# Kernel tuning notes

Measured on AMD Instinct MI355X. Metric: run time of the kernel, lower is better.

The kernel has to match this reference:

```python
import jax, jax.numpy as jnp
import numpy as np

B, C1, C2, K, H, W = 2, 256, 256, 3, 64, 64
PAD = 1
EPS = 1e-5
K2 = K * K
OUT_OFF = 3 * K2  # deform_groups=1: 2*k2 offset channels + k2 mask channels


def setup_inputs() -> dict:
    key = jax.random.key(0)
    ks = jax.random.split(key, 8)
    x = jax.random.normal(ks[0], (B, C1, H, W), jnp.float32)
    # small scale so predicted offsets stay within a few pixels (realistic trained regime)
    w_off = jax.random.normal(ks[1], (OUT_OFF, C1, 3, 3), jnp.float32) * 0.01
    b_off = jax.random.normal(ks[2], (OUT_OFF,), jnp.float32) * 0.01
    w_dcn = jax.random.normal(ks[3], (C2, C1, K, K), jnp.float32) / np.sqrt(C1 * K2).astype(np.float32)
    gamma = 1.0 + 0.1 * jax.random.normal(ks[4], (C2,), jnp.float32)
    beta = 0.1 * jax.random.normal(ks[5], (C2,), jnp.float32)
    run_mean = 0.1 * jax.random.normal(ks[6], (C2,), jnp.float32)
    run_var = jax.random.uniform(ks[7], (C2,), jnp.float32, minval=0.5, maxval=1.5)
    return {"x": x, "w_off": w_off, "b_off": b_off, "w_dcn": w_dcn,
            "gamma": gamma, "beta": beta, "run_mean": run_mean, "run_var": run_var}


def _dcnv2_bn_silu(x, w_off, b_off, w_dcn, gamma, beta, run_mean, run_var):
    # offset/mask predictor: plain 3x3 conv, stride 1, pad 1
    om = jax.lax.conv_general_dilated(x, w_off, (1, 1), [(PAD, PAD), (PAD, PAD)])
    om = om + b_off[None, :, None, None]  # [B, 27, H, W]
    # mmcv channel layout: (dy, dx) interleaved per kernel tap, then mask
    offset = om[:, :2 * K2].reshape(B, K2, 2, H, W)
    mask = jax.nn.sigmoid(om[:, 2 * K2:3 * K2])  # [B, K2, H, W]
    dy, dx = offset[:, :, 0], offset[:, :, 1]     # [B, K2, H, W]

    ki = jnp.arange(K)
    tap_y = jnp.repeat(ki, K)  # [K2]
    tap_x = jnp.tile(ki, K)    # [K2]
    base_y = jnp.arange(H)[None, None, :, None] - PAD + tap_y[None, :, None, None]
    base_x = jnp.arange(W)[None, None, None, :] - PAD + tap_x[None, :, None, None]
    py = base_y.astype(x.dtype) + dy  # [B, K2, H, W] sampling rows
    px = base_x.astype(x.dtype) + dx  # [B, K2, H, W] sampling cols

    y0f = jnp.floor(py)
    x0f = jnp.floor(px)
    ly = (py - y0f)[:, None]  # [B, 1, K2, H, W]
    lx = (px - x0f)[:, None]
    y0 = y0f.astype(jnp.int32)
    x0 = x0f.astype(jnp.int32)

    x_flat = x.reshape(B, C1, H * W)

    def gather(yi, xi):
        valid = ((yi >= 0) & (yi < H) & (xi >= 0) & (xi < W)).astype(x.dtype)
        idx = jnp.clip(yi, 0, H - 1) * W + jnp.clip(xi, 0, W - 1)  # [B, K2, H, W]
        v = jnp.take_along_axis(x_flat, idx.reshape(B, 1, -1), axis=2)
        return v.reshape(B, C1, K2, H, W) * valid[:, None]

    v00 = gather(y0, x0)
    v01 = gather(y0, x0 + 1)
    v10 = gather(y0 + 1, x0)
    v11 = gather(y0 + 1, x0 + 1)
    vals = (v00 * (1 - ly) * (1 - lx) + v01 * (1 - ly) * lx
            + v10 * ly * (1 - lx) + v11 * ly * lx)
    vals = vals * mask[:, None]  # modulated

    out = jnp.einsum('bckhw,ock->bohw', vals, w_dcn.reshape(C2, C1, K2))

    # BatchNorm (inference, running stats) + SiLU
    inv = gamma / jnp.sqrt(run_var + EPS)
    y = out * inv[None, :, None, None] + (beta - run_mean * inv)[None, :, None, None]
    return y * jax.nn.sigmoid(y)


def reference(x, w_off, b_off, w_dcn, gamma, beta, run_mean, run_var):
    return _dcnv2_bn_silu(x, w_off, b_off, w_dcn, gamma, beta, run_mean, run_var)
```

## Files before the change

kernel.cpp:

```cpp
#include <hip/hip_runtime.h>
#include <hip/hip_bf16.h>
#include <math.h>

typedef __bf16 bf16x8 __attribute__((ext_vector_type(8)));
typedef float  f32x4  __attribute__((ext_vector_type(4)));

#define BB 2
#define C1 256
#define C2 256
#define HH 64
#define WW 64
#define HW 4096
#define OCH 27
#define EPSV 1e-5f

#define WBF_OFF  0u
#define WOFF_OFF 1179648u
#define XT_OFF   1327104u

__global__ __launch_bounds__(256) void prep_kernel(
    const float* __restrict__ x, const float* __restrict__ w_dcn,
    const float* __restrict__ w_off, __bf16* __restrict__ xT,
    __bf16* __restrict__ wbfS, __bf16* __restrict__ woffS)
{
    __shared__ __bf16 tile[64][72];
    __shared__ __bf16 lw[16][584];
    const int bi = blockIdx.x, tid = threadIdx.x;

    if (bi < 512) {
        const int b = bi >> 8;
        const int ht = (bi & 255) >> 2;
        const int ct = bi & 3;
        const int hw_l = tid & 63, cg = tid >> 6;
        const float* src = x + ((size_t)(b * 256 + ct * 64 + cg * 16) << 12)
                             + ht * 64 + hw_l;
        #pragma unroll
        for (int i = 0; i < 16; i++)
            tile[hw_l][cg * 16 + i] = (__bf16)src[(size_t)i << 12];
        __syncthreads();
        const int hw_o = tid >> 2, cq = tid & 3;
        __bf16* dst = xT + ((size_t)(b * HW + ht * 64 + hw_o) << 8)
                         + ct * 64 + cq * 16;
        *(bf16x8*)dst       = *(const bf16x8*)&tile[hw_o][cq * 16];
        *(bf16x8*)(dst + 8) = *(const bf16x8*)&tile[hw_o][cq * 16 + 8];
    } else if (bi < 576) {
        const int b2 = bi - 512;
        const int nb = b2 >> 2, qtr = b2 & 3;
        #pragma unroll
        for (int ii = 0; ii < 9; ii++) {
            int m = tid + 256 * ii;
            int base = m * 4;
            int o_l = base / 576;
            int f = base - o_l * 576;
            float4 v = *(const float4*)(w_dcn
                + (size_t)(nb * 16 + o_l) * 2304 + qtr * 576 + f);
            lw[o_l][f]     = (__bf16)v.x;
            lw[o_l][f + 1] = (__bf16)v.y;
            lw[o_l][f + 2] = (__bf16)v.z;
            lw[o_l][f + 3] = (__bf16)v.w;
        }
        __syncthreads();
        for (int p = tid; p < 1152; p += 256) {
            int lane = p & 63, seg = p >> 6;
            int tap = seg >> 1, ks = seg & 1;
            int kb = tap * 4 + qtr;
            int o_l = lane & 15, kq = (lane >> 4) & 3;
            bf16x8 v;
            #pragma unroll
            for (int j = 0; j < 8; j++)
                v[j] = lw[o_l][(ks * 32 + kq * 8 + j) * 9 + tap];
            *(bf16x8*)(wbfS
                + ((size_t)(((kb * 2 + ks) * 16 + nb) * 64 + lane)) * 8) = v;
        }
    } else {
        int t = (bi - 576) * 256 + tid;
        int l = t & 63;
        int nf = (t >> 6) & 1;
        int ks = (t >> 7) & 1;
        int kb = t >> 8;
        int o = nf * 16 + (l & 15);
        int kq = (l >> 4) & 3;
        bf16x8 v;
        #pragma unroll
        for (int j = 0; j < 8; j++) {
            int K = kb * 64 + ks * 32 + kq * 8 + j;
            v[j] = (o < OCH) ? (__bf16)w_off[o * 2304 + (K & 255) * 9 + (K >> 8)]
                             : (__bf16)0.f;
        }
        *(bf16x8*)(woffS + (size_t)t * 8) = v;
    }
}

union SU {
    float sD[8][2][16][33];
    float sC[4][32][133];
};

__global__ __launch_bounds__(512, 2) void fused_kernel(
    const __bf16* __restrict__ xT, const __bf16* __restrict__ wbfS,
    const __bf16* __restrict__ woffS, const float* __restrict__ b_off,
    const float* __restrict__ gamma, const float* __restrict__ beta,
    const float* __restrict__ rmean, const float* __restrict__ rvar,
    float* __restrict__ out)
{
    __shared__ SU u;
    __shared__ float  sOm[32][33];
    __shared__ int4   sO[9][32];
    __shared__ float4 sW[9][32];

    const int tid = threadIdx.x, wv = tid >> 6, lane = tid & 63;
    const int g = (blockIdx.x & 7) * 32 + (blockIdx.x >> 3);
    const int pixBase = g * 32;
    const int b = pixBase >> 12;
    const int hwBase = pixBase & 4095;
    const int h = hwBase >> 6, w0 = hwBase & 63;
    const int n15 = lane & 15, q4 = lane >> 4;

    const int cc  = wv >> 1;
    const int ksw = wv & 1;
    const char* xb = (const char*)xT + ((size_t)b << 12) * 512;
    const int chOffB = (cc * 64 + ksw * 32 + q4 * 8) * 2;

    {
        f32x4 acc2[2][2];
        #pragma unroll
        for (int nf = 0; nf < 2; nf++)
            #pragma unroll
            for (int t = 0; t < 2; t++)
                acc2[nf][t] = (f32x4){0.f, 0.f, 0.f, 0.f};

        #pragma unroll
        for (int k = 0; k < 9; k++) {
            const int kb = k * 4 + cc;
            const int kh = k / 3, kw = k % 3;
            const int hh = h + kh - 1;
            const int hc = min(max(hh, 0), HH - 1);
            const bool vy = (hh >= 0) && (hh < HH);
            bf16x8 af[2];
            #pragma unroll
            for (int t = 0; t < 2; t++) {
                const int ww = w0 + t * 16 + n15 + kw - 1;
                const bool valid = vy && (ww >= 0) && (ww < WW);
                const int wc = min(max(ww, 0), WW - 1);
                af[t] = *(const bf16x8*)(xb + (size_t)(hc * WW + wc) * 512
                                            + chOffB);
                if (!valid) {
                    #pragma unroll
                    for (int j = 0; j < 8; j++) af[t][j] = (__bf16)0.f;
                }
            }
            #pragma unroll
            for (int nf = 0; nf < 2; nf++) {
                bf16x8 bfr = *(const bf16x8*)(woffS
                    + ((size_t)(((kb * 2 + ksw) * 2 + nf) * 64 + lane)) * 8);
                #pragma unroll
                for (int t = 0; t < 2; t++)
                    acc2[nf][t] = __builtin_amdgcn_mfma_f32_16x16x32_bf16(
                        af[t], bfr, acc2[nf][t], 0, 0, 0);
            }
        }
        #pragma unroll
        for (int nf = 0; nf < 2; nf++)
            #pragma unroll
            for (int t = 0; t < 2; t++)
                #pragma unroll
                for (int r = 0; r < 4; r++)
                    u.sD[wv][t][q4 * 4 + r][nf * 16 + n15] = acc2[nf][t][r];
    }
    __syncthreads();
    for (int t2 = tid; t2 < OCH * 32; t2 += 512) {
        int oc = t2 >> 5, p = t2 & 31;
        float s = b_off[oc];
        #pragma unroll
        for (int w = 0; w < 8; w++) s += u.sD[w][p >> 4][p & 15][oc];
        sOm[oc][p] = s;
    }
    __syncthreads();

    if (tid < 288) {
        int k = tid >> 5, p = tid & 31;
        float dy = sOm[2 * k][p];
        float dx = sOm[2 * k + 1][p];
        float mm = sOm[18 + k][p];
        mm = 1.f / (1.f + __expf(-mm));
        float py = (float)(h - 1 + k / 3) + dy;
        float px = (float)(w0 + p - 1 + k % 3) + dx;
        float y0f = floorf(py), x0f = floorf(px);
        float ly = py - y0f, lx = px - x0f;
        int y0 = (int)y0f, x0 = (int)x0f;
        int yc0 = min(max(y0, 0), HH - 1),     yc1 = min(max(y0 + 1, 0), HH - 1);
        int xc0 = min(max(x0, 0), WW - 1),     xc1 = min(max(x0 + 1, 0), WW - 1);
        float vy0 = (y0 >= 0 && y0 < HH) ? 1.f : 0.f;
        float vy1 = (y0 + 1 >= 0 && y0 + 1 < HH) ? 1.f : 0.f;
        float vx0 = (x0 >= 0 && x0 < WW) ? 1.f : 0.f;
        float vx1 = (x0 + 1 >= 0 && x0 + 1 < WW) ? 1.f : 0.f;
        sO[k][p] = (int4){(yc0 * WW + xc0) * 512, (yc0 * WW + xc1) * 512,
                          (yc1 * WW + xc0) * 512, (yc1 * WW + xc1) * 512};
        sW[k][p] = (float4){(1.f - ly) * (1.f - lx) * vy0 * vx0 * mm,
                            (1.f - ly) * lx         * vy0 * vx1 * mm,
                            ly         * (1.f - lx) * vy1 * vx0 * mm,
                            ly         * lx         * vy1 * vx1 * mm};
    }
    __syncthreads();

    f32x4 acc[2][16];
    #pragma unroll
    for (int t = 0; t < 2; t++)
        #pragma unroll
        for (int j = 0; j < 16; j++) acc[t][j] = (f32x4){0.f, 0.f, 0.f, 0.f};

    const char* base = xb + chOffB;
    for (int k = 0; k < 9; k++) {
        const int kb = k * 4 + cc;
        const int4   O0 = sO[k][n15],      O1 = sO[k][16 + n15];
        const float4 W0 = sW[k][n15],      W1 = sW[k][16 + n15];

        bf16x8 a00 = *(const bf16x8*)(base + O0.x);
        bf16x8 a01 = *(const bf16x8*)(base + O0.y);
        bf16x8 a10 = *(const bf16x8*)(base + O0.z);
        bf16x8 a11 = *(const bf16x8*)(base + O0.w);
        bf16x8 b00 = *(const bf16x8*)(base + O1.x);
        bf16x8 b01 = *(const bf16x8*)(base + O1.y);
        bf16x8 b10 = *(const bf16x8*)(base + O1.z);
        bf16x8 b11 = *(const bf16x8*)(base + O1.w);

        bf16x8 af0, af1;
        #pragma unroll
        for (int j = 0; j < 8; j++) {
            float v0 = W0.x * (float)a00[j] + W0.y * (float)a01[j]
                     + W0.z * (float)a10[j] + W0.w * (float)a11[j];
            float v1 = W1.x * (float)b00[j] + W1.y * (float)b01[j]
                     + W1.z * (float)b10[j] + W1.w * (float)b11[j];
            af0[j] = (__bf16)v0;
            af1[j] = (__bf16)v1;
        }

        #pragma unroll
        for (int hf = 0; hf < 2; hf++) {
            bf16x8 bfr[8];
            #pragma unroll
            for (int nb = 0; nb < 8; nb++)
                bfr[nb] = *(const bf16x8*)(wbfS
                    + ((size_t)(((kb * 2 + ksw) * 16 + hf * 8 + nb) * 64 + lane)) * 8);
            #pragma unroll
            for (int nb = 0; nb < 8; nb++) {
                acc[0][hf * 8 + nb] = __builtin_amdgcn_mfma_f32_16x16x32_bf16(
                    af0, bfr[nb], acc[0][hf * 8 + nb], 0, 0, 0);
                acc[1][hf * 8 + nb] = __builtin_amdgcn_mfma_f32_16x16x32_bf16(
                    af1, bfr[nb], acc[1][hf * 8 + nb], 0, 0, 0);
            }
        }
    }

    #pragma unroll
    for (int pass = 0; pass < 2; pass++) {
        if (wv < 4) {
            #pragma unroll
            for (int t = 0; t < 2; t++)
                #pragma unroll
                for (int nb = 0; nb < 8; nb++)
                    #pragma unroll
                    for (int r = 0; r < 4; r++)
                        u.sC[wv][t * 16 + q4 * 4 + r][nb * 16 + n15]
                            = acc[t][pass * 8 + nb][r];
        }
        __syncthreads();
        if (wv >= 4) {
            #pragma unroll
            for (int t = 0; t < 2; t++)
                #pragma unroll
                for (int nb = 0; nb < 8; nb++)
                    #pragma unroll
                    for (int r = 0; r < 4; r++)
                        u.sC[wv - 4][t * 16 + q4 * 4 + r][nb * 16 + n15]
                            += acc[t][pass * 8 + nb][r];
        }
        __syncthreads();

        const int px = tid & 31, og = tid >> 5;
        #pragma unroll
        for (int ii = 0; ii < 8; ii++) {
            int col = og * 8 + ii;
            int o = pass * 128 + col;
            float s = u.sC[0][px][col] + u.sC[1][px][col]
                    + u.sC[2][px][col] + u.sC[3][px][col];
            float inv = gamma[o] * rsqrtf(rvar[o] + EPSV);
            float sh = beta[o] - rmean[o] * inv;
            float y = s * inv + sh;
            out[(size_t)((b * C2 + o) << 12) + hwBase + px]
                = y * (1.f / (1.f + __expf(-y)));
        }
        __syncthreads();
    }
}

extern "C" void kernel_launch(void* const* d_in, const int* in_sizes, int n_in,
                              void* d_out, int out_size, void* d_ws, size_t ws_size,
                              hipStream_t stream) {
    const float* x      = (const float*)d_in[0];
    const float* w_off  = (const float*)d_in[1];
    const float* b_off  = (const float*)d_in[2];
    const float* w_dcn  = (const float*)d_in[3];
    const float* gamma  = (const float*)d_in[4];
    const float* beta   = (const float*)d_in[5];
    const float* rmean  = (const float*)d_in[6];
    const float* rvar   = (const float*)d_in[7];
    float* out = (float*)d_out;

    char* ws = (char*)d_ws;
    __bf16* wbfS  = (__bf16*)(ws + WBF_OFF);
    __bf16* woffS = (__bf16*)(ws + WOFF_OFF);
    __bf16* xT    = (__bf16*)(ws + XT_OFF);

    prep_kernel<<<612, 256, 0, stream>>>(x, w_dcn, w_off, xT, wbfS, woffS);
    fused_kernel<<<256, 512, 0, stream>>>(xT, wbfS, woffS, b_off,
                                          gamma, beta, rmean, rvar, out);
}
```

Measured before the change: 121.1 us.

## Merge prep and fused kernels into one cooperative kernel with grid sync

Combines the layout/precision prep kernel and the main deformable-conv kernel into a single cooperative launch. Each of the 256 blocks first transposes its share of x to bf16, and some blocks also repack the weights. A grid-wide barrier follows, then the original fused compute runs. This removes one kernel launch and the gap between the two kernels. In exchange it adds a grid sync, and it requires all 256 blocks of 512 threads to be co-resident, which the cooperative launch enforces.

```diff
diff --git a/kernel.cpp b/kernel.cpp
--- a/kernel.cpp
+++ b/kernel.cpp
@@ -1,6 +1,9 @@
 #include <hip/hip_runtime.h>
 #include <hip/hip_bf16.h>
+#include <hip/hip_cooperative_groups.h>
 #include <math.h>
+
+namespace cg = cooperative_groups;
 
 typedef __bf16 bf16x8 __attribute__((ext_vector_type(8)));
 typedef float  f32x4  __attribute__((ext_vector_type(4)));
@@ -18,62 +21,83 @@
 #define WOFF_OFF 1179648u
 #define XT_OFF   1327104u
 
-__global__ __launch_bounds__(256) void prep_kernel(
-    const float* __restrict__ x, const float* __restrict__ w_dcn,
-    const float* __restrict__ w_off, __bf16* __restrict__ xT,
+union SU {
+    float  sD[8][2][16][33];
+    float  sC[4][32][133];
+    __bf16 tile[2][64][72];
+    __bf16 lw[16][584];
+};
+
+__global__ __launch_bounds__(512, 2) void mega_kernel(
+    const float* __restrict__ x, const float* __restrict__ w_off,
+    const float* __restrict__ w_dcn, const float* __restrict__ b_off,
+    const float* __restrict__ gamma, const float* __restrict__ beta,
+    const float* __restrict__ rmean, const float* __restrict__ rvar,
+    float* __restrict__ out, __bf16* __restrict__ xT,
     __bf16* __restrict__ wbfS, __bf16* __restrict__ woffS)
 {
-    __shared__ __bf16 tile[64][72];
-    __shared__ __bf16 lw[16][584];
-    const int bi = blockIdx.x, tid = threadIdx.x;
-
-    if (bi < 512) {
-        const int b = bi >> 8;
-        const int ht = (bi & 255) >> 2;
-        const int ct = bi & 3;
-        const int hw_l = tid & 63, cg = tid >> 6;
+    __shared__ SU u;
+    __shared__ float  sOm[32][33];
+    __shared__ int4   sO[9][32];
+    __shared__ float4 sW[9][32];
+
+    const int tid = threadIdx.x, bid = blockIdx.x;
+
+    {
+        const int sub = tid >> 8, t8 = tid & 255;
+        const int u2 = bid * 2 + sub;
+        const int b = u2 >> 8;
+        const int ht = (u2 & 255) >> 2;
+        const int ct = u2 & 3;
+        const int hw_l = t8 & 63, cg = t8 >> 6;
         const float* src = x + ((size_t)(b * 256 + ct * 64 + cg * 16) << 12)
                              + ht * 64 + hw_l;
         #pragma unroll
         for (int i = 0; i < 16; i++)
-            tile[hw_l][cg * 16 + i] = (__bf16)src[(size_t)i << 12];
-        __syncthreads();
-        const int hw_o = tid >> 2, cq = tid & 3;
+            u.tile[sub][hw_l][cg * 16 + i] = (__bf16)src[(size_t)i << 12];
+        __syncthreads();
+        const int hw_o = t8 >> 2, cq = t8 & 3;
         __bf16* dst = xT + ((size_t)(b * HW + ht * 64 + hw_o) << 8)
                          + ct * 64 + cq * 16;
-        *(bf16x8*)dst       = *(const bf16x8*)&tile[hw_o][cq * 16];
-        *(bf16x8*)(dst + 8) = *(const bf16x8*)&tile[hw_o][cq * 16 + 8];
-    } else if (bi < 576) {
-        const int b2 = bi - 512;
-        const int nb = b2 >> 2, qtr = b2 & 3;
-        #pragma unroll
-        for (int ii = 0; ii < 9; ii++) {
-            int m = tid + 256 * ii;
-            int base = m * 4;
-            int o_l = base / 576;
-            int f = base - o_l * 576;
-            float4 v = *(const float4*)(w_dcn
-                + (size_t)(nb * 16 + o_l) * 2304 + qtr * 576 + f);
-            lw[o_l][f]     = (__bf16)v.x;
-            lw[o_l][f + 1] = (__bf16)v.y;
-            lw[o_l][f + 2] = (__bf16)v.z;
-            lw[o_l][f + 3] = (__bf16)v.w;
-        }
-        __syncthreads();
-        for (int p = tid; p < 1152; p += 256) {
-            int lane = p & 63, seg = p >> 6;
-            int tap = seg >> 1, ks = seg & 1;
-            int kb = tap * 4 + qtr;
-            int o_l = lane & 15, kq = (lane >> 4) & 3;
-            bf16x8 v;
-            #pragma unroll
-            for (int j = 0; j < 8; j++)
-                v[j] = lw[o_l][(ks * 32 + kq * 8 + j) * 9 + tap];
-            *(bf16x8*)(wbfS
-                + ((size_t)(((kb * 2 + ks) * 16 + nb) * 64 + lane)) * 8) = v;
-        }
-    } else {
-        int t = (bi - 576) * 256 + tid;
+        *(bf16x8*)dst       = *(const bf16x8*)&u.tile[sub][hw_o][cq * 16];
+        *(bf16x8*)(dst + 8) = *(const bf16x8*)&u.tile[sub][hw_o][cq * 16 + 8];
+    }
+    __syncthreads();
+
+    if (bid < 64) {
+        const int nb = bid >> 2, qtr = bid & 3;
+        if (tid < 256) {
+            #pragma unroll
+            for (int ii = 0; ii < 9; ii++) {
+                int m = tid + 256 * ii;
+                int base = m * 4;
+                int o_l = base / 576;
+                int f = base - o_l * 576;
+                float4 v = *(const float4*)(w_dcn
+                    + (size_t)(nb * 16 + o_l) * 2304 + qtr * 576 + f);
+                u.lw[o_l][f]     = (__bf16)v.x;
+                u.lw[o_l][f + 1] = (__bf16)v.y;
+                u.lw[o_l][f + 2] = (__bf16)v.z;
+                u.lw[o_l][f + 3] = (__bf16)v.w;
+            }
+        }
+        __syncthreads();
+        if (tid < 256) {
+            for (int p = tid; p < 1152; p += 256) {
+                int lane = p & 63, seg = p >> 6;
+                int tap = seg >> 1, ks = seg & 1;
+                int kb = tap * 4 + qtr;
+                int o_l = lane & 15, kq = (lane >> 4) & 3;
+                bf16x8 v;
+                #pragma unroll
+                for (int j = 0; j < 8; j++)
+                    v[j] = u.lw[o_l][(ks * 32 + kq * 8 + j) * 9 + tap];
+                *(bf16x8*)(wbfS
+                    + ((size_t)(((kb * 2 + ks) * 16 + nb) * 64 + lane)) * 8) = v;
+            }
+        }
+    } else if (bid < 82) {
+        int t = (bid - 64) * 512 + tid;
         int l = t & 63;
         int nf = (t >> 6) & 1;
         int ks = (t >> 7) & 1;
@@ -89,27 +113,14 @@
         }
         *(bf16x8*)(woffS + (size_t)t * 8) = v;
     }
-}
-
-union SU {
-    float sD[8][2][16][33];
-    float sC[4][32][133];
-};
-
-__global__ __launch_bounds__(512, 2) void fused_kernel(
-    const __bf16* __restrict__ xT, const __bf16* __restrict__ wbfS,
-    const __bf16* __restrict__ woffS, const float* __restrict__ b_off,
-    const float* __restrict__ gamma, const float* __restrict__ beta,
-    const float* __restrict__ rmean, const float* __restrict__ rvar,
-    float* __restrict__ out)
-{
-    __shared__ SU u;
-    __shared__ float  sOm[32][33];
-    __shared__ int4   sO[9][32];
-    __shared__ float4 sW[9][32];
-
-    const int tid = threadIdx.x, wv = tid >> 6, lane = tid & 63;
-    const int g = (blockIdx.x & 7) * 32 + (blockIdx.x >> 3);
+
+    __threadfence();
+    cg::this_grid().sync();
+    __threadfence();
+    __syncthreads();
+
+    const int wv = tid >> 6, lane = tid & 63;
+    const int g = (bid & 7) * 32 + (bid >> 3);
     const int pixBase = g * 32;
     const int b = pixBase >> 12;
     const int hwBase = pixBase & 4095;
@@ -312,7 +323,11 @@
     __bf16* woffS = (__bf16*)(ws + WOFF_OFF);
     __bf16* xT    = (__bf16*)(ws + XT_OFF);
 
-    prep_kernel<<<612, 256, 0, stream>>>(x, w_dcn, w_off, xT, wbfS, woffS);
-    fused_kernel<<<256, 512, 0, stream>>>(xT, wbfS, woffS, b_off,
-                                          gamma, beta, rmean, rvar, out);
+    void* args[] = {
+        (void*)&x, (void*)&w_off, (void*)&w_dcn, (void*)&b_off,
+        (void*)&gamma, (void*)&beta, (void*)&rmean, (void*)&rvar,
+        (void*)&out, (void*)&xT, (void*)&wbfS, (void*)&woffS
+    };
+    hipLaunchCooperativeKernel((const void*)mega_kernel, dim3(256), dim3(512),
+                               args, 0, stream);
 }
```

After: 260.1 us. 115% more time.
